# Kernel tuning notes

Hardware: AMD Instinct MI355X
Metric: run time of the kernel (lower is better)

The kernel has to match this reference:

```python
import jax, jax.numpy as jnp
import numpy as np

B, T, E, H, W = 2, 1024, 1024, 8, 31
D = 2 * W + 1  # head dim must equal 2*window_size+1 for the rel-pos broadcast


def _ln(x, w, b):
    mu = jnp.mean(x, axis=-1, keepdims=True)
    var = jnp.mean(jnp.square(x - mu), axis=-1, keepdims=True)
    return (x - mu) * jax.lax.rsqrt(var + 1e-5) * w + b


def setup_inputs() -> dict:
    key = jax.random.key(0)
    k = jax.random.split(key, 8)
    s = 0.02
    return {
        "x": jax.random.normal(k[0], (B, T, E // 2), jnp.float32),
        "ln1_w": jnp.ones(E, jnp.float32), "ln1_b": jnp.zeros(E, jnp.float32),
        "qkv_w": jax.random.normal(k[1], (3 * H * D, E), jnp.float32) * s,
        "qkv_b": jnp.zeros(3 * H * D, jnp.float32),
        "rel_pos": jax.random.normal(k[2], (D, D), jnp.float32) * s,
        "proj_w": jax.random.normal(k[3], (E, H * D), jnp.float32) * s,
        "proj_b": jnp.zeros(E, jnp.float32),
        "ln2_w": jnp.ones(E, jnp.float32), "ln2_b": jnp.zeros(E, jnp.float32),
        "fc_w": jax.random.normal(k[4], (4 * E, E), jnp.float32) * s,
        "fc_b": jnp.zeros(4 * E, jnp.float32),
        "cproj_w": jax.random.normal(k[5], (E, 4 * E), jnp.float32) * s,
        "cproj_b": jnp.zeros(E, jnp.float32),
    }


def reference(x, ln1_w, ln1_b, qkv_w, qkv_b, rel_pos, proj_w, proj_b,
              ln2_w, ln2_b, fc_w, fc_b, cproj_w, cproj_b):
    # --- RotaryEmbedding: angle = x * inv_freq; out = cat(sin, cos) -> [B,T,E]
    dim = 2 * x.shape[-1]
    inv_freq = 1.0 / 10000.0 ** (jnp.arange(0, dim, 2, dtype=jnp.float32) / dim)
    ang = x * inv_freq
    xr = jnp.concatenate([jnp.sin(ang), jnp.cos(ang)], axis=-1)  # [B,T,E]

    # --- custom windowed attention on ln_1(xr)
    h = _ln(xr, ln1_w, ln1_b)
    qkv = h @ qkv_w.T + qkv_b                       # [B,T,3*H*D]
    q, k, v = jnp.split(qkv, 3, axis=-1)

    def heads(t):
        return t.reshape(B, T, H, D).transpose(0, 2, 1, 3)  # [B,H,T,D]

    q, k, v = heads(q), heads(k), heads(v)
    # per-token q-outer-k scores (einsum '...bd,...bv->...bdv'): [B,H,T,D,D]
    scores = jnp.einsum('bhtd,bhtv->bhtdv', q, k)
    # rel-pos bias: Embedding lookup at offsets -W..W (negative indices wrap)
    bias = rel_pos[jnp.arange(-W, W + 1) % D]       # [D, D] == [2W+1, d_model]
    attn = jax.nn.softmax(scores + bias, axis=-2)   # softmax over non-canonical axis
    out = jnp.einsum('bhtdv,bhtv->bhtd', attn, v)   # apply per-token attn matrix to v
    out = out.transpose(0, 2, 1, 3).reshape(B, T, H * D)
    xa = xr + out @ proj_w.T + proj_b               # residual

    # --- MLP
    h2 = _ln(xa, ln2_w, ln2_b)
    m = jax.nn.gelu(h2 @ fc_w.T + fc_b, approximate=False) @ cproj_w.T + cproj_b
    return xa + m
```

## Files before the change

kernel.cpp:

```cpp
#include <hip/hip_runtime.h>
#include <hip/hip_bf16.h>


typedef __bf16 bf16;
typedef bf16 bf16x8 __attribute__((ext_vector_type(8)));
typedef bf16 bf16x4 __attribute__((ext_vector_type(4)));
typedef bf16 bf16x2 __attribute__((ext_vector_type(2)));
typedef float f32x4 __attribute__((ext_vector_type(4)));

__global__ __launch_bounds__(256) void rotary_ln_kernel(
    const float* __restrict__ x, const float* __restrict__ w,
    const float* __restrict__ b, float* __restrict__ xr, bf16* __restrict__ Y)
{
    const int row = blockIdx.x;
    const int tid = threadIdx.x;
    float2 xv = *(const float2*)(x + (size_t)row * 512 + tid * 2);
    float i0 = exp2f(-(float)(2*tid)     * 0.025952563241307518f);
    float i1 = exp2f(-(float)(2*tid + 1) * 0.025952563241307518f);
    float a0 = xv.x * i0, a1 = xv.y * i1;
    float s0 = sinf(a0), s1 = sinf(a1);
    float c0 = cosf(a0), c1 = cosf(a1);
    *(float2*)(xr + (size_t)row * 1024 + tid*2)       = make_float2(s0, s1);
    *(float2*)(xr + (size_t)row * 1024 + 512 + tid*2) = make_float2(c0, c1);
    float s  = s0 + s1 + c0 + c1;
    float ss = s0*s0 + s1*s1 + c0*c0 + c1*c1;
    #pragma unroll
    for (int off = 32; off > 0; off >>= 1) {
        s  += __shfl_down(s, off);
        ss += __shfl_down(ss, off);
    }
    __shared__ float rs[4], rss[4];
    int wave = tid >> 6, lane = tid & 63;
    if (lane == 0) { rs[wave] = s; rss[wave] = ss; }
    __syncthreads();
    s  = rs[0] + rs[1] + rs[2] + rs[3];
    ss = rss[0] + rss[1] + rss[2] + rss[3];
    float mu   = s * (1.f / 1024.f);
    float var  = ss * (1.f / 1024.f) - mu * mu;
    float rstd = rsqrtf(var + 1e-5f);
    float2 w0 = *(const float2*)(w + tid*2);
    float2 b0 = *(const float2*)(b + tid*2);
    float2 w1 = *(const float2*)(w + 512 + tid*2);
    float2 b1 = *(const float2*)(b + 512 + tid*2);
    bf16x2 y0, y1;
    y0[0] = (bf16)((s0 - mu) * rstd * w0.x + b0.x);
    y0[1] = (bf16)((s1 - mu) * rstd * w0.y + b0.y);
    y1[0] = (bf16)((c0 - mu) * rstd * w1.x + b1.x);
    y1[1] = (bf16)((c1 - mu) * rstd * w1.y + b1.y);
    *(bf16x2*)(Y + (size_t)row * 1024 + tid*2)       = y0;
    *(bf16x2*)(Y + (size_t)row * 1024 + 512 + tid*2) = y1;
}

__global__ __launch_bounds__(256) void ln_bf16_kernel(
    const float* __restrict__ X, const float* __restrict__ w,
    const float* __restrict__ b, bf16* __restrict__ Y)
{
    int row = blockIdx.x;
    const float4* xp = (const float4*)(X + (size_t)row * 1024);
    float4 xv = xp[threadIdx.x];
    float s  = xv.x + xv.y + xv.z + xv.w;
    float ss = xv.x*xv.x + xv.y*xv.y + xv.z*xv.z + xv.w*xv.w;
    #pragma unroll
    for (int off = 32; off > 0; off >>= 1) {
        s  += __shfl_down(s, off);
        ss += __shfl_down(ss, off);
    }
    __shared__ float rs[4], rss[4];
    int wave = threadIdx.x >> 6, lane = threadIdx.x & 63;
    if (lane == 0) { rs[wave] = s; rss[wave] = ss; }
    __syncthreads();
    s  = rs[0] + rs[1] + rs[2] + rs[3];
    ss = rss[0] + rss[1] + rss[2] + rss[3];
    float mu  = s * (1.f / 1024.f);
    float var = ss * (1.f / 1024.f) - mu * mu;
    float rstd = rsqrtf(var + 1e-5f);
    float4 wv = ((const float4*)w)[threadIdx.x];
    float4 bv = ((const float4*)b)[threadIdx.x];
    bf16 y[4];
    y[0] = (bf16)((xv.x - mu) * rstd * wv.x + bv.x);
    y[1] = (bf16)((xv.y - mu) * rstd * wv.y + bv.y);
    y[2] = (bf16)((xv.z - mu) * rstd * wv.z + bv.z);
    y[3] = (bf16)((xv.w - mu) * rstd * wv.w + bv.w);
    *(uint2*)(Y + (size_t)row * 1024 + threadIdx.x * 4) = *(uint2*)y;
}

__device__ __forceinline__ void conv_chunk(
    const float* __restrict__ src, bf16* __restrict__ dst,
    int ci, int N, int K, int Kp)
{
    int kpc = Kp >> 3;
    int r  = ci / kpc;
    int kc = (ci - r * kpc) << 3;
    bf16x8 o;
    if (r < N && kc < K) {
        float4 f0 = *(const float4*)(src + (size_t)r * K + kc);
        float4 f1 = *(const float4*)(src + (size_t)r * K + kc + 4);
        o[0]=(bf16)f0.x; o[1]=(bf16)f0.y; o[2]=(bf16)f0.z; o[3]=(bf16)f0.w;
        o[4]=(bf16)f1.x; o[5]=(bf16)f1.y; o[6]=(bf16)f1.z; o[7]=(bf16)f1.w;
    } else {
        #pragma unroll
        for (int j = 0; j < 8; ++j) o[j] = (bf16)0.f;
    }
    *(bf16x8*)(dst + (size_t)r * Kp + kc) = o;
}

__global__ __launch_bounds__(256) void conv_all_kernel(
    const float* __restrict__ qkv_w, const float* __restrict__ proj_w,
    const float* __restrict__ fc_w,  const float* __restrict__ cproj_w,
    const float* __restrict__ qkv_b,
    bf16* __restrict__ wqkv, bf16* __restrict__ wproj,
    bf16* __restrict__ wfc,  bf16* __restrict__ wcproj,
    float* __restrict__ qkvb_p)
{
    if (blockIdx.x == 5120) {
        for (int i = threadIdx.x; i < 1536; i += 256)
            qkvb_p[i] = (i < 1512) ? qkv_b[i] : 0.f;
        return;
    }
    int idx = blockIdx.x * 256 + threadIdx.x;
    if      (idx < 196608)  conv_chunk(qkv_w,   wqkv,   idx,          1512, 1024, 1024);
    else if (idx < 262144)  conv_chunk(proj_w,  wproj,  idx - 196608, 1024,  504,  512);
    else if (idx < 786432)  conv_chunk(fc_w,    wfc,    idx - 262144, 4096, 1024, 1024);
    else                    conv_chunk(cproj_w, wcproj, idx - 786432, 1024, 4096, 4096);
}

__device__ __forceinline__ float gelu_exact(float v)
{
    return 0.5f * v * (1.f + erff(v * 0.70710678118654752f));
}

template<int EPI>
__global__ __launch_bounds__(256, 4) void gemm6_kernel(
    const bf16* __restrict__ A, const bf16* __restrict__ Wt,
    const float* __restrict__ bias,
    float* Cf, bf16* Cb, int N, int Kp, int ksplit)
{
    __shared__ __align__(16) char lds[2][12288];

    const int tid  = threadIdx.x;
    const int w    = tid >> 6;
    const int lane = tid & 63;

    const int gx = gridDim.x, gy = gridDim.y;
    const int nwg = gx * gy * gridDim.z;
    const int chunk = nwg >> 3;
    int id = (blockIdx.z * gy + blockIdx.y) * gx + blockIdx.x;
    int sw = (id & 7) * chunk + (id >> 3);
    const int bx = sw % gx;
    const int t2 = sw / gx;
    const int by = t2 % gy;
    const int bz = t2 / gy;

    const int row0 = by * 64;
    const int col0 = bx * 128;
    const int wr = (w >> 1) * 32;
    const int wc = (w & 1) * 64;
    const int rl = lane & 15;
    const int kb16 = (lane >> 4) * 16;

    const size_t strideBy = (size_t)Kp * 2;
    const size_t kz = (size_t)bz * ksplit * 2;
    const char* Abase = (const char*)A  + (size_t)row0 * strideBy + kz;
    const char* Wbase = (const char*)Wt + (size_t)col0 * strideBy + kz;

    const size_t srcA0 = (size_t)(tid >> 2) * strideBy + (tid & 3) * 16;
    size_t srcB[2];
    #pragma unroll
    for (int i = 0; i < 2; ++i) {
        int o = (i * 256 + tid) * 16;
        srcB[i] = (size_t)(o >> 6) * strideBy + (o & 63);
    }

    f32x4 acc[2][4] = {};

    auto STAGE = [&](int buf, int kt) {
        const char* ab = Abase + (size_t)kt * 64;
        const char* wb = Wbase + (size_t)kt * 64;
        __builtin_amdgcn_global_load_lds(
            (const __attribute__((address_space(1))) void*)(ab + srcA0),
            (__attribute__((address_space(3))) void*)(&lds[buf][0] + tid * 16),
            16, 0, 0);
        #pragma unroll
        for (int i = 0; i < 2; ++i)
            __builtin_amdgcn_global_load_lds(
                (const __attribute__((address_space(1))) void*)(wb + srcB[i]),
                (__attribute__((address_space(3))) void*)(&lds[buf][4096] + (i*256 + tid)*16),
                16, 0, 0);
    };

    const int niter = ksplit >> 5;
    STAGE(0, 0);
    __syncthreads();
    for (int kt = 0; kt < niter; ++kt) {
        if (kt + 1 < niter)
            STAGE((kt + 1) & 1, kt + 1);
        const char* base = lds[kt & 1];
        bf16x8 af[2], bfr[4];
        #pragma unroll
        for (int mi = 0; mi < 2; ++mi)
            af[mi] = *(const bf16x8*)(base + ((wr + mi*16 + rl) << 6) + kb16);
        #pragma unroll
        for (int nj = 0; nj < 4; ++nj)
            bfr[nj] = *(const bf16x8*)(base + 4096 + ((wc + nj*16 + rl) << 6) + kb16);
        __builtin_amdgcn_s_setprio(1);
        #pragma unroll
        for (int mi = 0; mi < 2; ++mi)
            #pragma unroll
            for (int nj = 0; nj < 4; ++nj)
                acc[mi][nj] = __builtin_amdgcn_mfma_f32_16x16x32_bf16(
                    af[mi], bfr[nj], acc[mi][nj], 0, 0, 0);
        __builtin_amdgcn_s_setprio(0);
        __syncthreads();
    }

    const int rq = (lane >> 4) * 4;
    bf16* Cbz = Cb;
    if (EPI == 3) Cbz += (size_t)bz * 2048 * N;
    #pragma unroll
    for (int mi = 0; mi < 2; ++mi) {
        #pragma unroll
        for (int rj = 0; rj < 4; ++rj) {
            int row = row0 + wr + mi*16 + rq + rj;
            #pragma unroll
            for (int nj = 0; nj < 4; ++nj) {
                int col = col0 + wc + nj*16 + rl;
                float c = acc[mi][nj][rj];
                if (EPI != 3) c += bias[col];
                size_t off = (size_t)row * N + col;
                if (EPI == 0)      Cb[off]  = (bf16)c;
                else if (EPI == 1) Cb[off]  = (bf16)gelu_exact(c);
                else               Cbz[off] = (bf16)c;
            }
        }
    }
}

template<int P>
__global__ __launch_bounds__(256) void reduce_kernel(
    const bf16* __restrict__ parts, const float* __restrict__ bias,
    const float* R, float* out)
{
    int row = blockIdx.x;
    int c = threadIdx.x * 4;
    size_t off = (size_t)row * 1024 + c;
    float4 bv = *(const float4*)(bias + c);
    float4 o = *(const float4*)(R + off);
    o.x += bv.x; o.y += bv.y; o.z += bv.z; o.w += bv.w;
    #pragma unroll
    for (int p = 0; p < P; ++p) {
        bf16x4 v = *(const bf16x4*)(parts + (size_t)p * 2048 * 1024 + off);
        o.x += (float)v[0]; o.y += (float)v[1];
        o.z += (float)v[2]; o.w += (float)v[3];
    }
    *(float4*)(out + off) = o;
}

__global__ __launch_bounds__(256) void attn_kernel(
    const bf16* __restrict__ qkv, const float* __restrict__ rel_pos,
    bf16* __restrict__ outp)
{
    __shared__ float sbias[64*65];
    __shared__ float kmw[4][3][64];
    for (int i = threadIdx.x; i < 63*63; i += 256) {
        int d = i / 63, v = i - d*63;
        sbias[d*65 + v] = rel_pos[((d + 32) % 63) * 63 + v];
    }
    __syncthreads();
    const int wave = threadIdx.x >> 6;
    const int lane = threadIdx.x & 63;
    const int tk  = blockIdx.x * 4 + wave;
    const int row = tk >> 3;
    const int h   = tk & 7;
    const bf16* base = qkv + (size_t)row * 1536 + h * 63;
    float q_own = 0.f, k_own = 0.f, v_own = 0.f;
    if (lane < 63) {
        q_own = (float)base[lane];
        k_own = (float)base[504 + lane];
        v_own = (float)base[1008 + lane];
    }
    float m = -1e30f;
    for (int d = 0; d < 63; ++d) {
        float qd = __shfl(q_own, d);
        m = fmaxf(m, fmaf(qd, k_own, sbias[d*65 + lane]));
    }
    float Z = 0.f;
    for (int d = 0; d < 63; ++d) {
        float qd = __shfl(q_own, d);
        Z += __expf(fmaf(qd, k_own, sbias[d*65 + lane]) - m);
    }
    kmw[wave][0][lane] = k_own;
    kmw[wave][1][lane] = m;
    kmw[wave][2][lane] = v_own / Z;
    float acc = 0.f;
    for (int v = 0; v < 63; ++v) {
        float s = fmaf(q_own, kmw[wave][0][v], sbias[lane*65 + v]) - kmw[wave][1][v];
        acc += __expf(s) * kmw[wave][2][v];
    }
    if (lane < 63)
        outp[(size_t)row * 512 + h*63 + lane] = (bf16)acc;
    if (h == 7 && lane == 63) {
        #pragma unroll
        for (int j = 0; j < 8; ++j)
            outp[(size_t)row * 512 + 504 + j] = (bf16)0.f;
    }
}

extern "C" void kernel_launch(void* const* d_in, const int* in_sizes, int n_in,
                              void* d_out, int out_size, void* d_ws, size_t ws_size,
                              hipStream_t stream)
{
    const float* x       = (const float*)d_in[0];
    const float* ln1_w   = (const float*)d_in[1];
    const float* ln1_b   = (const float*)d_in[2];
    const float* qkv_w   = (const float*)d_in[3];
    const float* qkv_b   = (const float*)d_in[4];
    const float* rel_pos = (const float*)d_in[5];
    const float* proj_w  = (const float*)d_in[6];
    const float* proj_b  = (const float*)d_in[7];
    const float* ln2_w   = (const float*)d_in[8];
    const float* ln2_b   = (const float*)d_in[9];
    const float* fc_w    = (const float*)d_in[10];
    const float* fc_b    = (const float*)d_in[11];
    const float* cproj_w = (const float*)d_in[12];
    const float* cproj_b = (const float*)d_in[13];
    float* out = (float*)d_out;

    char* p = (char*)d_ws;
    float* xr      = (float*)p;            p += (size_t)2048*1024*4;
    bf16*  h_bf    = (bf16*)p;             p += (size_t)2048*1024*2;
    bf16*  wqkv    = (bf16*)p;             p += (size_t)1536*1024*2;
    bf16*  wproj   = (bf16*)p;             p += (size_t)1024*512*2;
    bf16*  wfc     = (bf16*)p;             p += (size_t)4096*1024*2;
    bf16*  wcproj  = (bf16*)p;             p += (size_t)1024*4096*2;
    float* qkvb_p  = (float*)p;            p += 8192;
    bf16*  attn_bf = (bf16*)p;             p += (size_t)2048*512*2;
    bf16*  qkvb    = (bf16*)p;
    bf16*  fc_act  = (bf16*)p;
    bf16*  proj_part = qkvb;
    bf16*  cp_part = (bf16*)d_ws;

    conv_all_kernel<<<5121, 256, 0, stream>>>(qkv_w, proj_w, fc_w, cproj_w, qkv_b,
                                              wqkv, wproj, wfc, wcproj, qkvb_p);
    rotary_ln_kernel<<<2048, 256, 0, stream>>>(x, ln1_w, ln1_b, xr, h_bf);
    gemm6_kernel<0><<<dim3(12,32,1), 256, 0, stream>>>(h_bf, wqkv, qkvb_p,
                                                       nullptr, qkvb, 1536, 1024, 1024);
    attn_kernel<<<4096, 256, 0, stream>>>(qkvb, rel_pos, attn_bf);
    gemm6_kernel<3><<<dim3(8,32,2), 256, 0, stream>>>(attn_bf, wproj, nullptr,
                                                      nullptr, proj_part, 1024, 512, 256);
    reduce_kernel<2><<<2048, 256, 0, stream>>>(proj_part, proj_b, xr, out);
    ln_bf16_kernel<<<2048, 256, 0, stream>>>(out, ln2_w, ln2_b, h_bf);
    gemm6_kernel<1><<<dim3(32,32,1), 256, 0, stream>>>(h_bf, wfc, fc_b,
                                                       nullptr, fc_act, 4096, 1024, 1024);
    gemm6_kernel<3><<<dim3(8,32,4), 256, 0, stream>>>(fc_act, wcproj, nullptr,
                                                      nullptr, cp_part, 1024, 4096, 1024);
    reduce_kernel<4><<<2048, 256, 0, stream>>>(cp_part, cproj_b, out, out);
}
```

Before: 152.9 us.

## Add larger-tile 512-thread GEMM with swizzled LDS and triple-buffered B for MLP

Adds a new GEMM kernel with 128x256 tiles, 8 waves, a K-step of 64, XOR-swizzled LDS layout, double-buffered A and triple-buffered B, with explicit vmcnt waits and raw barriers. It replaces the old GEMM for the MLP fc and cproj matmuls. The goal is more data reuse per block, fewer LDS bank conflicts and deeper prefetch. In exchange the kernel uses 128KB of LDS and launches fewer workgroups (256 for fc, 256 for cproj), which lowers occupancy and may leave CUs underused.

```diff
diff --git a/kernel.cpp b/kernel.cpp
--- a/kernel.cpp
+++ b/kernel.cpp
@@ -124,22 +124,48 @@
     else                    conv_chunk(cproj_w, wcproj, idx - 786432, 1024, 4096, 4096);
 }
 
+template<int N> __device__ __forceinline__ void vmwait()
+{
+    if constexpr      (N==0) asm volatile("s_waitcnt vmcnt(0)" ::: "memory");
+    else if constexpr (N==4) asm volatile("s_waitcnt vmcnt(4)" ::: "memory");
+    else if constexpr (N==6) asm volatile("s_waitcnt vmcnt(6)" ::: "memory");
+}
+__device__ __forceinline__ void lgkmwait0()
+{
+    asm volatile("s_waitcnt lgkmcnt(0)" ::: "memory");
+}
+__device__ __forceinline__ void hw_barrier()
+{
+    asm volatile("s_barrier" ::: "memory");
+}
+
+__device__ __forceinline__ void gload16(const char* src, char* ldsdst)
+{
+    __builtin_amdgcn_global_load_lds(
+        (const __attribute__((address_space(1))) void*)src,
+        (__attribute__((address_space(3))) void*)ldsdst, 16, 0, 0);
+}
+
 __device__ __forceinline__ float gelu_exact(float v)
 {
     return 0.5f * v * (1.f + erff(v * 0.70710678118654752f));
 }
 
 template<int EPI>
-__global__ __launch_bounds__(256, 4) void gemm6_kernel(
+__global__ __launch_bounds__(512, 2) void gemm8_kernel(
     const bf16* __restrict__ A, const bf16* __restrict__ Wt,
-    const float* __restrict__ bias,
-    float* Cf, bf16* Cb, int N, int Kp, int ksplit)
-{
-    __shared__ __align__(16) char lds[2][12288];
+    const float* __restrict__ bias, bf16* __restrict__ Cb,
+    int N, int Kp, int ksplit)
+{
+    __shared__ __align__(16) char lds[131072];
 
     const int tid  = threadIdx.x;
     const int w    = tid >> 6;
     const int lane = tid & 63;
+    const int wm   = w >> 2;
+    const int wn   = w & 3;
+    const int rl   = lane & 15;
+    const int lh   = lane >> 4;
 
     const int gx = gridDim.x, gy = gridDim.y;
     const int nwg = gx * gy * gridDim.z;
@@ -151,6 +177,138 @@
     const int by = t2 % gy;
     const int bz = t2 / gy;
 
+    const int row0 = by * 128;
+    const int col0 = bx * 256;
+    const size_t strideBy = (size_t)Kp * 2;
+    const size_t kz = (size_t)bz * ksplit * 2;
+    const char* Abase = (const char*)A  + (size_t)row0 * strideBy + kz;
+    const char* Wbase = (const char*)Wt + (size_t)col0 * strideBy + kz;
+
+    size_t srcA[2], srcB[4];
+    #pragma unroll
+    for (int i = 0; i < 2; ++i) {
+        int ls = i * 512 + tid;
+        int r = ls >> 3, s = ls & 7;
+        srcA[i] = (size_t)r * strideBy + (size_t)((s ^ (r & 7)) << 4);
+    }
+    #pragma unroll
+    for (int i = 0; i < 4; ++i) {
+        int ls = i * 512 + tid;
+        int r = ls >> 3, s = ls & 7;
+        srcB[i] = (size_t)r * strideBy + (size_t)((s ^ (r & 7)) << 4);
+    }
+
+    auto STAGE_A = [&](int buf, int kt) {
+        const char* ab = Abase + (size_t)kt * 128;
+        char* d = &lds[buf * 16384];
+        #pragma unroll
+        for (int i = 0; i < 2; ++i)
+            gload16(ab + srcA[i], d + (i * 512 + tid) * 16);
+    };
+    auto STAGE_B = [&](int buf, int kt) {
+        const char* wb = Wbase + (size_t)kt * 128;
+        char* d = &lds[32768 + buf * 32768];
+        #pragma unroll
+        for (int i = 0; i < 4; ++i)
+            gload16(wb + srcB[i], d + (i * 512 + tid) * 16);
+    };
+
+    f32x4 acc[4][4] = {};
+    const int niter = ksplit >> 6;
+
+    STAGE_A(0, 0);
+    STAGE_B(0, 0);
+    STAGE_B(1, 1);
+    vmwait<4>();
+    hw_barrier();
+
+    int cb3 = 0, sb3 = 2;
+    for (int kt = 0; kt < niter; ++kt) {
+        if (kt + 1 < niter) STAGE_A((kt + 1) & 1, kt + 1);
+        if (kt + 2 < niter) STAGE_B(sb3, kt + 2);
+
+        const char* pA = &lds[(kt & 1) * 16384];
+        const char* pB = &lds[32768 + cb3 * 32768];
+        bf16x8 af[4][2], bq[4][2];
+        #pragma unroll
+        for (int mi = 0; mi < 4; ++mi) {
+            int ar = wm * 64 + mi * 16 + rl;
+            #pragma unroll
+            for (int ks = 0; ks < 2; ++ks)
+                af[mi][ks] = *(const bf16x8*)
+                    (pA + ar * 128 + (((ks * 4 + lh) ^ (ar & 7)) << 4));
+        }
+        #pragma unroll
+        for (int nj = 0; nj < 4; ++nj) {
+            int br = wn * 64 + nj * 16 + rl;
+            #pragma unroll
+            for (int ks = 0; ks < 2; ++ks)
+                bq[nj][ks] = *(const bf16x8*)
+                    (pB + br * 128 + (((ks * 4 + lh) ^ (br & 7)) << 4));
+        }
+        __builtin_amdgcn_s_setprio(1);
+        #pragma unroll
+        for (int ks = 0; ks < 2; ++ks)
+            #pragma unroll
+            for (int mi = 0; mi < 4; ++mi)
+                #pragma unroll
+                for (int nj = 0; nj < 4; ++nj)
+                    acc[mi][nj] = __builtin_amdgcn_mfma_f32_16x16x32_bf16(
+                        af[mi][ks], bq[nj][ks], acc[mi][nj], 0, 0, 0);
+        __builtin_amdgcn_s_setprio(0);
+
+        if (kt + 1 < niter) {
+            lgkmwait0();
+            if (kt + 2 < niter) vmwait<4>();
+            else                vmwait<0>();
+            hw_barrier();
+        }
+        cb3 = (cb3 == 2) ? 0 : cb3 + 1;
+        sb3 = (sb3 == 2) ? 0 : sb3 + 1;
+    }
+
+    const int rq = lh * 4;
+    bf16* Cbz = Cb;
+    if (EPI == 3) Cbz += (size_t)bz * 2048 * N;
+    #pragma unroll
+    for (int mi = 0; mi < 4; ++mi) {
+        #pragma unroll
+        for (int rj = 0; rj < 4; ++rj) {
+            int row = row0 + wm * 64 + mi * 16 + rq + rj;
+            #pragma unroll
+            for (int nj = 0; nj < 4; ++nj) {
+                int col = col0 + wn * 64 + nj * 16 + rl;
+                float c = acc[mi][nj][rj];
+                size_t off = (size_t)row * N + col;
+                if (EPI == 1) Cbz[off] = (bf16)gelu_exact(c + bias[col]);
+                else          Cbz[off] = (bf16)c;
+            }
+        }
+    }
+}
+
+template<int EPI>
+__global__ __launch_bounds__(256, 4) void gemm6_kernel(
+    const bf16* __restrict__ A, const bf16* __restrict__ Wt,
+    const float* __restrict__ bias,
+    float* Cf, bf16* Cb, int N, int Kp, int ksplit)
+{
+    __shared__ __align__(16) char lds[2][12288];
+
+    const int tid  = threadIdx.x;
+    const int w    = tid >> 6;
+    const int lane = tid & 63;
+
+    const int gx = gridDim.x, gy = gridDim.y;
+    const int nwg = gx * gy * gridDim.z;
+    const int chunk = nwg >> 3;
+    int id = (blockIdx.z * gy + blockIdx.y) * gx + blockIdx.x;
+    int sw = (id & 7) * chunk + (id >> 3);
+    const int bx = sw % gx;
+    const int t2 = sw / gx;
+    const int by = t2 % gy;
+    const int bz = t2 / gy;
+
     const int row0 = by * 64;
     const int col0 = bx * 128;
     const int wr = (w >> 1) * 32;
@@ -176,16 +334,10 @@
     auto STAGE = [&](int buf, int kt) {
         const char* ab = Abase + (size_t)kt * 64;
         const char* wb = Wbase + (size_t)kt * 64;
-        __builtin_amdgcn_global_load_lds(
-            (const __attribute__((address_space(1))) void*)(ab + srcA0),
-            (__attribute__((address_space(3))) void*)(&lds[buf][0] + tid * 16),
-            16, 0, 0);
+        gload16(ab + srcA0, &lds[buf][0] + tid * 16);
         #pragma unroll
         for (int i = 0; i < 2; ++i)
-            __builtin_amdgcn_global_load_lds(
-                (const __attribute__((address_space(1))) void*)(wb + srcB[i]),
-                (__attribute__((address_space(3))) void*)(&lds[buf][4096] + (i*256 + tid)*16),
-                16, 0, 0);
+            gload16(wb + srcB[i], &lds[buf][4096] + (i * 256 + tid) * 16);
     };
 
     const int niter = ksplit >> 5;
@@ -228,7 +380,6 @@
                 if (EPI != 3) c += bias[col];
                 size_t off = (size_t)row * N + col;
                 if (EPI == 0)      Cb[off]  = (bf16)c;
-                else if (EPI == 1) Cb[off]  = (bf16)gelu_exact(c);
                 else               Cbz[off] = (bf16)c;
             }
         }
@@ -349,9 +500,9 @@
                                                       nullptr, proj_part, 1024, 512, 256);
     reduce_kernel<2><<<2048, 256, 0, stream>>>(proj_part, proj_b, xr, out);
     ln_bf16_kernel<<<2048, 256, 0, stream>>>(out, ln2_w, ln2_b, h_bf);
-    gemm6_kernel<1><<<dim3(32,32,1), 256, 0, stream>>>(h_bf, wfc, fc_b,
-                                                       nullptr, fc_act, 4096, 1024, 1024);
-    gemm6_kernel<3><<<dim3(8,32,4), 256, 0, stream>>>(fc_act, wcproj, nullptr,
-                                                      nullptr, cp_part, 1024, 4096, 1024);
+    gemm8_kernel<1><<<dim3(16,16,1), 512, 0, stream>>>(h_bf, wfc, fc_b,
+                                                       fc_act, 4096, 1024, 1024);
+    gemm8_kernel<3><<<dim3(4,16,4), 512, 0, stream>>>(fc_act, wcproj, nullptr,
+                                                      cp_part, 1024, 4096, 1024);
     reduce_kernel<4><<<2048, 256, 0, stream>>>(cp_part, cproj_b, out, out);
 }
```

Result: faster. 145.0 us (-5.2%).

## Shrink GEMM tiles to 64x64 with XOR-swizzled LDS layout and higher occupancy

Applied to the files above, without the earlier changes.

Replaces the 64x128-tile GEMM with a 64x64-tile variant that uses half the LDS per block and declares 8 blocks per CU. It also applies an XOR swizzle to the 16-byte slot within each LDS row to cut bank conflicts on the fragment reads. Launch grids double in the N dimension to match. The aim is more blocks in flight and fewer LDS conflicts, at the cost of less operand reuse per block and more global traffic for the A operand.

```diff
diff --git a/kernel.cpp b/kernel.cpp
--- a/kernel.cpp
+++ b/kernel.cpp
@@ -124,22 +124,32 @@
     else                    conv_chunk(cproj_w, wcproj, idx - 786432, 1024, 4096, 4096);
 }
 
+__device__ __forceinline__ void gload16(const char* src, char* ldsdst)
+{
+    __builtin_amdgcn_global_load_lds(
+        (const __attribute__((address_space(1))) void*)src,
+        (__attribute__((address_space(3))) void*)ldsdst, 16, 0, 0);
+}
 __device__ __forceinline__ float gelu_exact(float v)
 {
     return 0.5f * v * (1.f + erff(v * 0.70710678118654752f));
 }
 
 template<int EPI>
-__global__ __launch_bounds__(256, 4) void gemm6_kernel(
+__global__ __launch_bounds__(256, 8) void gemmS_kernel(
     const bf16* __restrict__ A, const bf16* __restrict__ Wt,
-    const float* __restrict__ bias,
-    float* Cf, bf16* Cb, int N, int Kp, int ksplit)
-{
-    __shared__ __align__(16) char lds[2][12288];
+    const float* __restrict__ bias, bf16* __restrict__ Cb,
+    int N, int Kp, int ksplit)
+{
+    __shared__ __align__(16) char lds[2][8192];
 
     const int tid  = threadIdx.x;
     const int w    = tid >> 6;
     const int lane = tid & 63;
+    const int wm   = w >> 1;
+    const int wn   = w & 1;
+    const int rl   = lane & 15;
+    const int slotR = lane >> 4;
 
     const int gx = gridDim.x, gy = gridDim.y;
     const int nwg = gx * gy * gridDim.z;
@@ -152,40 +162,24 @@
     const int bz = t2 / gy;
 
     const int row0 = by * 64;
-    const int col0 = bx * 128;
-    const int wr = (w >> 1) * 32;
-    const int wc = (w & 1) * 64;
-    const int rl = lane & 15;
-    const int kb16 = (lane >> 4) * 16;
-
+    const int col0 = bx * 64;
     const size_t strideBy = (size_t)Kp * 2;
     const size_t kz = (size_t)bz * ksplit * 2;
     const char* Abase = (const char*)A  + (size_t)row0 * strideBy + kz;
     const char* Wbase = (const char*)Wt + (size_t)col0 * strideBy + kz;
 
-    const size_t srcA0 = (size_t)(tid >> 2) * strideBy + (tid & 3) * 16;
-    size_t srcB[2];
-    #pragma unroll
-    for (int i = 0; i < 2; ++i) {
-        int o = (i * 256 + tid) * 16;
-        srcB[i] = (size_t)(o >> 6) * strideBy + (o & 63);
-    }
-
-    f32x4 acc[2][4] = {};
+    const int srow  = tid >> 2;
+    const int sslot = tid & 3;
+    const size_t srcOff = (size_t)srow * strideBy
+                        + (size_t)((sslot ^ ((srow >> 1) & 3)) << 4);
+
+    f32x4 acc[2][2] = {};
 
     auto STAGE = [&](int buf, int kt) {
         const char* ab = Abase + (size_t)kt * 64;
         const char* wb = Wbase + (size_t)kt * 64;
-        __builtin_amdgcn_global_load_lds(
-            (const __attribute__((address_space(1))) void*)(ab + srcA0),
-            (__attribute__((address_space(3))) void*)(&lds[buf][0] + tid * 16),
-            16, 0, 0);
-        #pragma unroll
-        for (int i = 0; i < 2; ++i)
-            __builtin_amdgcn_global_load_lds(
-                (const __attribute__((address_space(1))) void*)(wb + srcB[i]),
-                (__attribute__((address_space(3))) void*)(&lds[buf][4096] + (i*256 + tid)*16),
-                16, 0, 0);
+        gload16(ab + srcOff, &lds[buf][0]    + tid * 16);
+        gload16(wb + srcOff, &lds[buf][4096] + tid * 16);
     };
 
     const int niter = ksplit >> 5;
@@ -195,18 +189,24 @@
         if (kt + 1 < niter)
             STAGE((kt + 1) & 1, kt + 1);
         const char* base = lds[kt & 1];
-        bf16x8 af[2], bfr[4];
-        #pragma unroll
-        for (int mi = 0; mi < 2; ++mi)
-            af[mi] = *(const bf16x8*)(base + ((wr + mi*16 + rl) << 6) + kb16);
-        #pragma unroll
-        for (int nj = 0; nj < 4; ++nj)
-            bfr[nj] = *(const bf16x8*)(base + 4096 + ((wc + nj*16 + rl) << 6) + kb16);
+        bf16x8 af[2], bfr[2];
+        #pragma unroll
+        for (int mi = 0; mi < 2; ++mi) {
+            int r = wm * 32 + mi * 16 + rl;
+            af[mi] = *(const bf16x8*)
+                (base + r * 64 + ((slotR ^ ((r >> 1) & 3)) << 4));
+        }
+        #pragma unroll
+        for (int nj = 0; nj < 2; ++nj) {
+            int r = wn * 32 + nj * 16 + rl;
+            bfr[nj] = *(const bf16x8*)
+                (base + 4096 + r * 64 + ((slotR ^ ((r >> 1) & 3)) << 4));
+        }
         __builtin_amdgcn_s_setprio(1);
         #pragma unroll
         for (int mi = 0; mi < 2; ++mi)
             #pragma unroll
-            for (int nj = 0; nj < 4; ++nj)
+            for (int nj = 0; nj < 2; ++nj)
                 acc[mi][nj] = __builtin_amdgcn_mfma_f32_16x16x32_bf16(
                     af[mi], bfr[nj], acc[mi][nj], 0, 0, 0);
         __builtin_amdgcn_s_setprio(0);
@@ -220,15 +220,14 @@
     for (int mi = 0; mi < 2; ++mi) {
         #pragma unroll
         for (int rj = 0; rj < 4; ++rj) {
-            int row = row0 + wr + mi*16 + rq + rj;
+            int row = row0 + wm * 32 + mi * 16 + rq + rj;
             #pragma unroll
-            for (int nj = 0; nj < 4; ++nj) {
-                int col = col0 + wc + nj*16 + rl;
+            for (int nj = 0; nj < 2; ++nj) {
+                int col = col0 + wn * 32 + nj * 16 + rl;
                 float c = acc[mi][nj][rj];
-                if (EPI != 3) c += bias[col];
                 size_t off = (size_t)row * N + col;
-                if (EPI == 0)      Cb[off]  = (bf16)c;
-                else if (EPI == 1) Cb[off]  = (bf16)gelu_exact(c);
+                if (EPI == 0)      Cbz[off] = (bf16)(c + bias[col]);
+                else if (EPI == 1) Cbz[off] = (bf16)gelu_exact(c + bias[col]);
                 else               Cbz[off] = (bf16)c;
             }
         }
@@ -342,16 +341,16 @@
     conv_all_kernel<<<5121, 256, 0, stream>>>(qkv_w, proj_w, fc_w, cproj_w, qkv_b,
                                               wqkv, wproj, wfc, wcproj, qkvb_p);
     rotary_ln_kernel<<<2048, 256, 0, stream>>>(x, ln1_w, ln1_b, xr, h_bf);
-    gemm6_kernel<0><<<dim3(12,32,1), 256, 0, stream>>>(h_bf, wqkv, qkvb_p,
-                                                       nullptr, qkvb, 1536, 1024, 1024);
+    gemmS_kernel<0><<<dim3(24,32,1), 256, 0, stream>>>(h_bf, wqkv, qkvb_p,
+                                                       qkvb, 1536, 1024, 1024);
     attn_kernel<<<4096, 256, 0, stream>>>(qkvb, rel_pos, attn_bf);
-    gemm6_kernel<3><<<dim3(8,32,2), 256, 0, stream>>>(attn_bf, wproj, nullptr,
-                                                      nullptr, proj_part, 1024, 512, 256);
+    gemmS_kernel<3><<<dim3(16,32,2), 256, 0, stream>>>(attn_bf, wproj, nullptr,
+                                                       proj_part, 1024, 512, 256);
     reduce_kernel<2><<<2048, 256, 0, stream>>>(proj_part, proj_b, xr, out);
     ln_bf16_kernel<<<2048, 256, 0, stream>>>(out, ln2_w, ln2_b, h_bf);
-    gemm6_kernel<1><<<dim3(32,32,1), 256, 0, stream>>>(h_bf, wfc, fc_b,
-                                                       nullptr, fc_act, 4096, 1024, 1024);
-    gemm6_kernel<3><<<dim3(8,32,4), 256, 0, stream>>>(fc_act, wcproj, nullptr,
-                                                      nullptr, cp_part, 1024, 4096, 1024);
+    gemmS_kernel<1><<<dim3(64,32,1), 256, 0, stream>>>(h_bf, wfc, fc_b,
+                                                       fc_act, 4096, 1024, 1024);
+    gemmS_kernel<3><<<dim3(16,32,4), 256, 0, stream>>>(fc_act, wcproj, nullptr,
+                                                       cp_part, 1024, 4096, 1024);
     reduce_kernel<4><<<2048, 256, 0, stream>>>(cp_part, cproj_b, out, out);
 }
```

After: 171.9 us. 12.4% more time.
